# Performance work log

Measured on AMD Instinct MI355X. Metric: run time of the kernel, lower is better.

The kernel has to match this reference:

```python
import jax, jax.numpy as jnp
import numpy as np

EMB_DIM = 1024
HEAD_SIZE = 64
SEQ = 2048
BATCH = 8


def setup_inputs() -> dict:
    key = jax.random.key(0)
    kx, kq, kk, kv = jax.random.split(key, 4)
    x = jax.random.normal(kx, (BATCH, SEQ, EMB_DIM), dtype=jnp.float32)
    # nn.Linear(E, H, bias=False): y = x @ W.T with W of shape [H, E]; store as [E, H]
    s = 1.0 / np.sqrt(EMB_DIM)
    Wq = jax.random.uniform(kq, (EMB_DIM, HEAD_SIZE), jnp.float32, -s, s)
    Wk = jax.random.uniform(kk, (EMB_DIM, HEAD_SIZE), jnp.float32, -s, s)
    Wv = jax.random.uniform(kv, (EMB_DIM, HEAD_SIZE), jnp.float32, -s, s)
    return {"x": x, "Wq": Wq, "Wk": Wk, "Wv": Wv}


def reference(x, Wq, Wk, Wv):
    B, S, E = x.shape
    q = jnp.einsum("bse,eh->bsh", x, Wq)
    k = jnp.einsum("bse,eh->bsh", x, Wk)
    v = jnp.einsum("bse,eh->bsh", x, Wv)
    # NOTE: original scales by E**-0.5 (embedding dim), not head_size**-0.5
    att = jnp.einsum("bqh,bkh->bqk", q, k) * (E ** -0.5)
    causal = jnp.tril(jnp.ones((S, S), dtype=bool))
    att = jnp.where(causal, att, -jnp.inf)
    att = jax.nn.softmax(att, axis=-1)
    # dropout(p=0.2) treated as identity (eval mode) for deterministic reference
    out = jnp.einsum("bqk,bkh->bqh", att, v)
    return out
```

## Files before the change

### kernel.cpp

```cpp
#include <hip/hip_runtime.h>

constexpr int Bn = 8, S = 2048, E = 1024, H = 64;
constexpr float SCALE = 0.03125f * 1.44269504f;

typedef __attribute__((ext_vector_type(8))) short short8;
typedef __attribute__((ext_vector_type(4))) float f32x4;

__device__ __forceinline__ unsigned short f2bf(float f) {
  unsigned u = __builtin_bit_cast(unsigned, f);
  u += 0x7fffu + ((u >> 16) & 1u);
  return (unsigned short)(u >> 16);
}
__device__ __forceinline__ ushort4 f4bf(float4 f) {
  return make_ushort4(f2bf(f.x), f2bf(f.y), f2bf(f.z), f2bf(f.w));
}

__global__ __launch_bounds__(256) void wtrans_kernel(
    const float* __restrict__ Wq, const float* __restrict__ Wk,
    const float* __restrict__ Wv, unsigned short* __restrict__ WT3) {
  __shared__ unsigned short tb[64][72];
  const int m = blockIdx.x >> 4;
  const int e0 = (blockIdx.x & 15) * 64;
  const float* W = (m == 0) ? Wq : (m == 1) ? Wk : Wv;
  const int t = threadIdx.x;
#pragma unroll
  for (int it = 0; it < 4; ++it) {
    int idx = t + it * 256;
    int r = idx >> 4, c4 = idx & 15;
    float4 f = ((const float4*)(W + (long)(e0 + r) * H))[c4];
    *(ushort4*)&tb[r][c4 * 4] = f4bf(f);
  }
  __syncthreads();
#pragma unroll
  for (int it = 0; it < 4; ++it) {
    int idx = t + it * 256;
    int h = idx >> 4, e4 = idx & 15;
    ushort4 u = make_ushort4(tb[e4 * 4 + 0][h], tb[e4 * 4 + 1][h],
                             tb[e4 * 4 + 2][h], tb[e4 * 4 + 3][h]);
    ((ushort4*)(WT3 + (long)(m * 64 + h) * E + e0))[e4] = u;
  }
}

__global__ __launch_bounds__(256) void qkv_kernel(
    const float* __restrict__ x, const unsigned short* __restrict__ WT3,
    unsigned short* __restrict__ q, unsigned short* __restrict__ kk,
    unsigned short* __restrict__ vT) {
  __shared__ unsigned short xs[32][136];
  __shared__ unsigned short ws[192][136];
  const int t = threadIdx.x;
  const int w = t >> 6, lane = t & 63, l15 = lane & 15, g = lane >> 4;
  const long row0 = (long)blockIdx.x * 32;
  const int xrow = t >> 5, xslot = t & 31;
  const int wrow = t >> 4, wslot = t & 15;

  f32x4 acc[2][3];
#pragma unroll
  for (int rt = 0; rt < 2; ++rt)
#pragma unroll
    for (int ct = 0; ct < 3; ++ct) acc[rt][ct] = f32x4{0.f, 0.f, 0.f, 0.f};

  float4 px[4];
  short8 pw[12];
#pragma unroll
  for (int it = 0; it < 4; ++it)
    px[it] = ((const float4*)(x + (row0 + xrow + it * 8) * E))[xslot];
#pragma unroll
  for (int it = 0; it < 12; ++it)
    pw[it] = *(const short8*)(WT3 + (long)(wrow + it * 16) * E + wslot * 8);
#pragma unroll
  for (int it = 0; it < 4; ++it)
    *(ushort4*)&xs[xrow + it * 8][xslot * 4] = f4bf(px[it]);
#pragma unroll
  for (int it = 0; it < 12; ++it)
    *(short8*)&ws[wrow + it * 16][wslot * 8] = pw[it];

  for (int c = 0; c < 8; ++c) {
    __syncthreads();
    if (c < 7) {
      const int e0 = (c + 1) * 128;
#pragma unroll
      for (int it = 0; it < 4; ++it)
        px[it] = ((const float4*)(x + (row0 + xrow + it * 8) * E + e0))[xslot];
#pragma unroll
      for (int it = 0; it < 12; ++it)
        pw[it] = *(const short8*)(WT3 + (long)(wrow + it * 16) * E + e0 + wslot * 8);
    }
#pragma unroll
    for (int kh = 0; kh < 4; ++kh) {
      short8 a0 = *(const short8*)&xs[l15][kh * 32 + g * 8];
      short8 a1 = *(const short8*)&xs[16 + l15][kh * 32 + g * 8];
#pragma unroll
      for (int ct = 0; ct < 3; ++ct) {
        short8 b = *(const short8*)&ws[w * 48 + ct * 16 + l15][kh * 32 + g * 8];
        acc[0][ct] = __builtin_amdgcn_mfma_f32_16x16x32_bf16(a0, b, acc[0][ct], 0, 0, 0);
        acc[1][ct] = __builtin_amdgcn_mfma_f32_16x16x32_bf16(a1, b, acc[1][ct], 0, 0, 0);
      }
    }
    __syncthreads();
    if (c < 7) {
#pragma unroll
      for (int it = 0; it < 4; ++it)
        *(ushort4*)&xs[xrow + it * 8][xslot * 4] = f4bf(px[it]);
#pragma unroll
      for (int it = 0; it < 12; ++it)
        *(short8*)&ws[wrow + it * 16][wslot * 8] = pw[it];
    }
  }

  const int bb = (int)(row0 >> 11);
  const int srow = (int)(row0 & 2047);
#pragma unroll
  for (int ct = 0; ct < 3; ++ct) {
    const int col = w * 48 + ct * 16 + l15;
    const int mm = col >> 6, ch = col & 63;
#pragma unroll
    for (int rt = 0; rt < 2; ++rt) {
      const int srl = rt * 16 + g * 4;
      if (mm == 0) {
#pragma unroll
        for (int r = 0; r < 4; ++r)
          q[(row0 + srl + r) * H + ch] = f2bf(acc[rt][ct][r] * SCALE);
      } else if (mm == 1) {
#pragma unroll
        for (int r = 0; r < 4; ++r)
          kk[(row0 + srl + r) * H + ch] = f2bf(acc[rt][ct][r]);
      } else {
        ushort4 v4 = make_ushort4(f2bf(acc[rt][ct][0]), f2bf(acc[rt][ct][1]),
                                  f2bf(acc[rt][ct][2]), f2bf(acc[rt][ct][3]));
        *(ushort4*)(vT + ((long)bb * H + ch) * S + srow + srl) = v4;
      }
    }
  }
}

__global__ __launch_bounds__(256, 2) void attn_kernel(
    const unsigned short* __restrict__ q, const unsigned short* __restrict__ k,
    const unsigned short* __restrict__ vT, float* __restrict__ out) {
  __shared__ unsigned short pl[4][16][72];
  __shared__ float Om[2][4][64][17];
  __shared__ float ms[2][4][16], ls[2][4][16];
  const int t = threadIdx.x;
  const int w = t >> 6, lane = t & 63, l15 = lane & 15, g = lane >> 4;
  const int b = blockIdx.x & 7, p = blockIdx.x >> 3;
  const unsigned short* kb = k + (long)b * S * H;
  const unsigned short* vb = vT + (long)b * H * S;

  const int qt0 = p, qt1 = 127 - p;
  const int nt0 = (qt0 >> 2) + 1;
  const int nt1 = (qt1 >> 2) + 1;
  const int qtA[2] = {qt0, qt1};
  const int ntA[2] = {nt0, nt1};
  const int k0A[2] = {w, (w + 4 - (nt0 & 3)) & 3};

  short8 bq0[2], bq1[2];
  f32x4 O[2][4];
  float m_[2], l_[2];
#pragma unroll
  for (int ph = 0; ph < 2; ++ph) {
    const unsigned short* qp = q + ((long)b * S + qtA[ph] * 16 + l15) * H + g * 8;
    bq0[ph] = *(const short8*)qp;
    bq1[ph] = *(const short8*)(qp + 32);
    m_[ph] = -1e30f;
    l_[ph] = 0.f;
#pragma unroll
    for (int c = 0; c < 4; ++c) O[ph][c] = f32x4{0.f, 0.f, 0.f, 0.f};
  }

#pragma unroll
  for (int ph = 0; ph < 2; ++ph) {
    const int qrow0 = qtA[ph] * 16;
    const int ntp = ntA[ph];
    short8 ak[4][2];
    int kt = k0A[ph];
    if (kt < ntp) {
#pragma unroll
      for (int c = 0; c < 4; ++c)
#pragma unroll
        for (int kh = 0; kh < 2; ++kh)
          ak[c][kh] = *(const short8*)(kb + (long)(kt * 64 + c * 16 + l15) * H + kh * 32 + g * 8);
    }
    for (; kt < ntp; kt += 4) {
      short8 av[4][2];
#pragma unroll
      for (int c = 0; c < 4; ++c)
#pragma unroll
        for (int kh = 0; kh < 2; ++kh)
          av[c][kh] = *(const short8*)(vb + (long)(c * 16 + l15) * S + kt * 64 + kh * 32 + g * 8);
      f32x4 sc[4];
#pragma unroll
      for (int c = 0; c < 4; ++c) {
        sc[c] = f32x4{0.f, 0.f, 0.f, 0.f};
        sc[c] = __builtin_amdgcn_mfma_f32_16x16x32_bf16(ak[c][0], bq0[ph], sc[c], 0, 0, 0);
        sc[c] = __builtin_amdgcn_mfma_f32_16x16x32_bf16(ak[c][1], bq1[ph], sc[c], 0, 0, 0);
      }
      if (kt + 4 < ntp) {
#pragma unroll
        for (int c = 0; c < 4; ++c)
#pragma unroll
          for (int kh = 0; kh < 2; ++kh)
            ak[c][kh] = *(const short8*)(kb + (long)((kt + 4) * 64 + c * 16 + l15) * H + kh * 32 + g * 8);
      }
      if (kt == ntp - 1) {
#pragma unroll
        for (int c = 0; c < 4; ++c)
#pragma unroll
          for (int r = 0; r < 4; ++r)
            if (kt * 64 + c * 16 + g * 4 + r > qrow0 + l15) sc[c][r] = -1e30f;
      }
      float mx = -1e30f;
#pragma unroll
      for (int c = 0; c < 4; ++c)
#pragma unroll
        for (int r = 0; r < 4; ++r) mx = fmaxf(mx, sc[c][r]);
      mx = fmaxf(mx, __shfl_xor(mx, 16));
      mx = fmaxf(mx, __shfl_xor(mx, 32));
      float mn = fmaxf(m_[ph], mx);
      float al = exp2f(m_[ph] - mn);
      float sum = 0.f;
#pragma unroll
      for (int c = 0; c < 4; ++c)
#pragma unroll
        for (int r = 0; r < 4; ++r) {
          float pe = exp2f(sc[c][r] - mn);
          sc[c][r] = pe;
          sum += pe;
        }
      sum += __shfl_xor(sum, 16);
      sum += __shfl_xor(sum, 32);
      l_[ph] = l_[ph] * al + sum;
      m_[ph] = mn;
#pragma unroll
      for (int c = 0; c < 4; ++c) {
        ushort4 p4 = make_ushort4(f2bf(sc[c][0]), f2bf(sc[c][1]),
                                  f2bf(sc[c][2]), f2bf(sc[c][3]));
        *(ushort4*)&pl[w][l15][c * 16 + g * 4] = p4;
      }
#pragma unroll
      for (int c = 0; c < 4; ++c)
#pragma unroll
        for (int r = 0; r < 4; ++r) O[ph][c][r] *= al;
      short8 bp0 = *(const short8*)&pl[w][l15][g * 8];
      short8 bp1 = *(const short8*)&pl[w][l15][32 + g * 8];
#pragma unroll
      for (int c = 0; c < 4; ++c) {
        O[ph][c] = __builtin_amdgcn_mfma_f32_16x16x32_bf16(av[c][0], bp0, O[ph][c], 0, 0, 0);
        O[ph][c] = __builtin_amdgcn_mfma_f32_16x16x32_bf16(av[c][1], bp1, O[ph][c], 0, 0, 0);
      }
    }
  }

#pragma unroll
  for (int ph = 0; ph < 2; ++ph) {
#pragma unroll
    for (int c = 0; c < 4; ++c)
#pragma unroll
      for (int r = 0; r < 4; ++r)
        Om[ph][w][c * 16 + g * 4 + r][l15] = O[ph][c][r];
    if (g == 0) { ms[ph][w][l15] = m_[ph]; ls[ph][w][l15] = l_[ph]; }
  }
  __syncthreads();
  if (w < 2) {
    const int ph = w;
    float mm0 = ms[ph][0][l15], mm1 = ms[ph][1][l15];
    float mm2 = ms[ph][2][l15], mm3 = ms[ph][3][l15];
    float mstar = fmaxf(fmaxf(mm0, mm1), fmaxf(mm2, mm3));
    float f0 = exp2f(mm0 - mstar), f1 = exp2f(mm1 - mstar);
    float f2 = exp2f(mm2 - mstar), f3 = exp2f(mm3 - mstar);
    float inv = 1.0f / (ls[ph][0][l15] * f0 + ls[ph][1][l15] * f1 +
                        ls[ph][2][l15] * f2 + ls[ph][3][l15] * f3);
    float* op = out + ((long)b * S + qtA[ph] * 16 + l15) * H;
#pragma unroll
    for (int c = 0; c < 4; ++c) {
      float o4[4];
#pragma unroll
      for (int r = 0; r < 4; ++r) {
        const int h = c * 16 + g * 4 + r;
        o4[r] = (Om[ph][0][h][l15] * f0 + Om[ph][1][h][l15] * f1 +
                 Om[ph][2][h][l15] * f2 + Om[ph][3][h][l15] * f3) * inv;
      }
      *(float4*)(op + c * 16 + g * 4) = make_float4(o4[0], o4[1], o4[2], o4[3]);
    }
  }
}

extern "C" void kernel_launch(void* const* d_in, const int* in_sizes, int n_in,
                              void* d_out, int out_size, void* d_ws, size_t ws_size,
                              hipStream_t stream) {
  const float* x  = (const float*)d_in[0];
  const float* Wq = (const float*)d_in[1];
  const float* Wk = (const float*)d_in[2];
  const float* Wv = (const float*)d_in[3];
  float* outp = (float*)d_out;
  unsigned short* WT3 = (unsigned short*)d_ws;
  unsigned short* q  = (unsigned short*)((char*)d_ws + 512 * 1024);
  unsigned short* kk = q + (size_t)Bn * S * H;
  unsigned short* vT = kk + (size_t)Bn * S * H;
  wtrans_kernel<<<dim3(48), dim3(256), 0, stream>>>(Wq, Wk, Wv, WT3);
  qkv_kernel<<<dim3((Bn * S) / 32), dim3(256), 0, stream>>>(x, WT3, q, kk, vT);
  attn_kernel<<<dim3(Bn * 64), dim3(256), 0, stream>>>(q, kk, vT, outp);
}
```

Baseline: 141.4 us.

## Process 32-row query groups per wave to reuse K/V loads, combine via LDS atomics

New measurement: 154.4 us. +9.2%, slower.

```diff
diff --git a/kernel.cpp b/kernel.cpp
--- a/kernel.cpp
+++ b/kernel.cpp
@@ -133,79 +133,78 @@
   }
 }
 
-__global__ __launch_bounds__(256, 2) void attn_kernel(
+__global__ __launch_bounds__(512, 2) void attn_kernel(
     const unsigned short* __restrict__ q, const unsigned short* __restrict__ k,
     const unsigned short* __restrict__ vT, float* __restrict__ out) {
-  __shared__ unsigned short pl[4][16][72];
-  __shared__ float Om[2][4][64][17];
-  __shared__ float ms[2][4][16], ls[2][4][16];
+  __shared__ unsigned short pl[8][16][72];
+  __shared__ float Oacc[2][32][68];
+  __shared__ float ms[2][4][32], ls[2][4][32];
   const int t = threadIdx.x;
   const int w = t >> 6, lane = t & 63, l15 = lane & 15, g = lane >> 4;
+  const int grp = w >> 2, w4 = w & 3;
   const int b = blockIdx.x & 7, p = blockIdx.x >> 3;
+  const int qg = grp ? (63 - p) : p;
+  const int nt = (qg >> 1) + 1;
+  const int qrow0 = qg * 32;
   const unsigned short* kb = k + (long)b * S * H;
   const unsigned short* vb = vT + (long)b * H * S;
 
-  const int qt0 = p, qt1 = 127 - p;
-  const int nt0 = (qt0 >> 2) + 1;
-  const int nt1 = (qt1 >> 2) + 1;
-  const int qtA[2] = {qt0, qt1};
-  const int ntA[2] = {nt0, nt1};
-  const int k0A[2] = {w, (w + 4 - (nt0 & 3)) & 3};
-
-  short8 bq0[2], bq1[2];
+  for (int i = t; i < 2 * 32 * 68; i += 512) ((float*)Oacc)[i] = 0.f;
+
+  short8 bq[2][2];
+#pragma unroll
+  for (int s = 0; s < 2; ++s) {
+    const unsigned short* qp = q + ((long)b * S + qrow0 + s * 16 + l15) * H + g * 8;
+    bq[s][0] = *(const short8*)qp;
+    bq[s][1] = *(const short8*)(qp + 32);
+  }
   f32x4 O[2][4];
-  float m_[2], l_[2];
-#pragma unroll
-  for (int ph = 0; ph < 2; ++ph) {
-    const unsigned short* qp = q + ((long)b * S + qtA[ph] * 16 + l15) * H + g * 8;
-    bq0[ph] = *(const short8*)qp;
-    bq1[ph] = *(const short8*)(qp + 32);
-    m_[ph] = -1e30f;
-    l_[ph] = 0.f;
-#pragma unroll
-    for (int c = 0; c < 4; ++c) O[ph][c] = f32x4{0.f, 0.f, 0.f, 0.f};
-  }
-
-#pragma unroll
-  for (int ph = 0; ph < 2; ++ph) {
-    const int qrow0 = qtA[ph] * 16;
-    const int ntp = ntA[ph];
-    short8 ak[4][2];
-    int kt = k0A[ph];
-    if (kt < ntp) {
-#pragma unroll
-      for (int c = 0; c < 4; ++c)
-#pragma unroll
-        for (int kh = 0; kh < 2; ++kh)
-          ak[c][kh] = *(const short8*)(kb + (long)(kt * 64 + c * 16 + l15) * H + kh * 32 + g * 8);
-    }
-    for (; kt < ntp; kt += 4) {
-      short8 av[4][2];
-#pragma unroll
-      for (int c = 0; c < 4; ++c)
-#pragma unroll
-        for (int kh = 0; kh < 2; ++kh)
-          av[c][kh] = *(const short8*)(vb + (long)(c * 16 + l15) * S + kt * 64 + kh * 32 + g * 8);
+  float m_[2] = {-1e30f, -1e30f}, l_[2] = {0.f, 0.f};
+#pragma unroll
+  for (int s = 0; s < 2; ++s)
+#pragma unroll
+    for (int c = 0; c < 4; ++c) O[s][c] = f32x4{0.f, 0.f, 0.f, 0.f};
+
+  short8 ak[4][2];
+  int kt = w4;
+  if (kt < nt) {
+#pragma unroll
+    for (int c = 0; c < 4; ++c)
+#pragma unroll
+      for (int kh = 0; kh < 2; ++kh)
+        ak[c][kh] = *(const short8*)(kb + (long)(kt * 64 + c * 16 + l15) * H + kh * 32 + g * 8);
+  }
+
+  for (; kt < nt; kt += 4) {
+    short8 av[4][2];
+#pragma unroll
+    for (int c = 0; c < 4; ++c)
+#pragma unroll
+      for (int kh = 0; kh < 2; ++kh)
+        av[c][kh] = *(const short8*)(vb + (long)(c * 16 + l15) * S + kt * 64 + kh * 32 + g * 8);
+    const bool last = (kt == nt - 1);
+#pragma unroll
+    for (int s = 0; s < 2; ++s) {
       f32x4 sc[4];
 #pragma unroll
       for (int c = 0; c < 4; ++c) {
         sc[c] = f32x4{0.f, 0.f, 0.f, 0.f};
-        sc[c] = __builtin_amdgcn_mfma_f32_16x16x32_bf16(ak[c][0], bq0[ph], sc[c], 0, 0, 0);
-        sc[c] = __builtin_amdgcn_mfma_f32_16x16x32_bf16(ak[c][1], bq1[ph], sc[c], 0, 0, 0);
-      }
-      if (kt + 4 < ntp) {
+        sc[c] = __builtin_amdgcn_mfma_f32_16x16x32_bf16(ak[c][0], bq[s][0], sc[c], 0, 0, 0);
+        sc[c] = __builtin_amdgcn_mfma_f32_16x16x32_bf16(ak[c][1], bq[s][1], sc[c], 0, 0, 0);
+      }
+      if (s == 1 && kt + 4 < nt) {
 #pragma unroll
         for (int c = 0; c < 4; ++c)
 #pragma unroll
           for (int kh = 0; kh < 2; ++kh)
             ak[c][kh] = *(const short8*)(kb + (long)((kt + 4) * 64 + c * 16 + l15) * H + kh * 32 + g * 8);
       }
-      if (kt == ntp - 1) {
+      if (last) {
 #pragma unroll
         for (int c = 0; c < 4; ++c)
 #pragma unroll
           for (int r = 0; r < 4; ++r)
-            if (kt * 64 + c * 16 + g * 4 + r > qrow0 + l15) sc[c][r] = -1e30f;
+            if (kt * 64 + c * 16 + g * 4 + r > qrow0 + s * 16 + l15) sc[c][r] = -1e30f;
       }
       float mx = -1e30f;
 #pragma unroll
@@ -214,8 +213,8 @@
         for (int r = 0; r < 4; ++r) mx = fmaxf(mx, sc[c][r]);
       mx = fmaxf(mx, __shfl_xor(mx, 16));
       mx = fmaxf(mx, __shfl_xor(mx, 32));
-      float mn = fmaxf(m_[ph], mx);
-      float al = exp2f(m_[ph] - mn);
+      float mn = fmaxf(m_[s], mx);
+      float al = exp2f(m_[s] - mn);
       float sum = 0.f;
 #pragma unroll
       for (int c = 0; c < 4; ++c)
@@ -227,8 +226,8 @@
         }
       sum += __shfl_xor(sum, 16);
       sum += __shfl_xor(sum, 32);
-      l_[ph] = l_[ph] * al + sum;
-      m_[ph] = mn;
+      l_[s] = l_[s] * al + sum;
+      m_[s] = mn;
 #pragma unroll
       for (int c = 0; c < 4; ++c) {
         ushort4 p4 = make_ushort4(f2bf(sc[c][0]), f2bf(sc[c][1]),
@@ -238,48 +237,56 @@
 #pragma unroll
       for (int c = 0; c < 4; ++c)
 #pragma unroll
-        for (int r = 0; r < 4; ++r) O[ph][c][r] *= al;
+        for (int r = 0; r < 4; ++r) O[s][c][r] *= al;
       short8 bp0 = *(const short8*)&pl[w][l15][g * 8];
       short8 bp1 = *(const short8*)&pl[w][l15][32 + g * 8];
 #pragma unroll
       for (int c = 0; c < 4; ++c) {
-        O[ph][c] = __builtin_amdgcn_mfma_f32_16x16x32_bf16(av[c][0], bp0, O[ph][c], 0, 0, 0);
-        O[ph][c] = __builtin_amdgcn_mfma_f32_16x16x32_bf16(av[c][1], bp1, O[ph][c], 0, 0, 0);
-      }
-    }
-  }
-
-#pragma unroll
-  for (int ph = 0; ph < 2; ++ph) {
+        O[s][c] = __builtin_amdgcn_mfma_f32_16x16x32_bf16(av[c][0], bp0, O[s][c], 0, 0, 0);
+        O[s][c] = __builtin_amdgcn_mfma_f32_16x16x32_bf16(av[c][1], bp1, O[s][c], 0, 0, 0);
+      }
+    }
+  }
+
+  if (g == 0) {
+    ms[grp][w4][l15]      = m_[0];  ls[grp][w4][l15]      = l_[0];
+    ms[grp][w4][16 + l15] = m_[1];  ls[grp][w4][16 + l15] = l_[1];
+  }
+  __syncthreads();
+#pragma unroll
+  for (int s = 0; s < 2; ++s) {
+    const int row = s * 16 + l15;
+    float mm0 = ms[grp][0][row], mm1 = ms[grp][1][row];
+    float mm2 = ms[grp][2][row], mm3 = ms[grp][3][row];
+    float mstar = fmaxf(fmaxf(mm0, mm1), fmaxf(mm2, mm3));
+    float f = exp2f(m_[s] - mstar);
 #pragma unroll
     for (int c = 0; c < 4; ++c)
 #pragma unroll
       for (int r = 0; r < 4; ++r)
-        Om[ph][w][c * 16 + g * 4 + r][l15] = O[ph][c][r];
-    if (g == 0) { ms[ph][w][l15] = m_[ph]; ls[ph][w][l15] = l_[ph]; }
+        atomicAdd(&Oacc[grp][row][c * 16 + g * 4 + r], O[s][c][r] * f);
   }
   __syncthreads();
-  if (w < 2) {
-    const int ph = w;
-    float mm0 = ms[ph][0][l15], mm1 = ms[ph][1][l15];
-    float mm2 = ms[ph][2][l15], mm3 = ms[ph][3][l15];
+  {
+    const int g2 = t >> 8, t256 = t & 255;
+    const int row = t256 >> 3, h0 = (t256 & 7) * 8;
+    const int qgo = g2 ? (63 - p) : p;
+    float mm0 = ms[g2][0][row], mm1 = ms[g2][1][row];
+    float mm2 = ms[g2][2][row], mm3 = ms[g2][3][row];
     float mstar = fmaxf(fmaxf(mm0, mm1), fmaxf(mm2, mm3));
-    float f0 = exp2f(mm0 - mstar), f1 = exp2f(mm1 - mstar);
-    float f2 = exp2f(mm2 - mstar), f3 = exp2f(mm3 - mstar);
-    float inv = 1.0f / (ls[ph][0][l15] * f0 + ls[ph][1][l15] * f1 +
-                        ls[ph][2][l15] * f2 + ls[ph][3][l15] * f3);
-    float* op = out + ((long)b * S + qtA[ph] * 16 + l15) * H;
-#pragma unroll
-    for (int c = 0; c < 4; ++c) {
-      float o4[4];
-#pragma unroll
-      for (int r = 0; r < 4; ++r) {
-        const int h = c * 16 + g * 4 + r;
-        o4[r] = (Om[ph][0][h][l15] * f0 + Om[ph][1][h][l15] * f1 +
-                 Om[ph][2][h][l15] * f2 + Om[ph][3][h][l15] * f3) * inv;
-      }
-      *(float4*)(op + c * 16 + g * 4) = make_float4(o4[0], o4[1], o4[2], o4[3]);
-    }
+    float lsum = ls[g2][0][row] * exp2f(mm0 - mstar) +
+                 ls[g2][1][row] * exp2f(mm1 - mstar) +
+                 ls[g2][2][row] * exp2f(mm2 - mstar) +
+                 ls[g2][3][row] * exp2f(mm3 - mstar);
+    float inv = 1.0f / lsum;
+    float* op = out + ((long)b * S + qgo * 32 + row) * H + h0;
+    float4 o0, o1;
+    o0.x = Oacc[g2][row][h0 + 0] * inv;  o0.y = Oacc[g2][row][h0 + 1] * inv;
+    o0.z = Oacc[g2][row][h0 + 2] * inv;  o0.w = Oacc[g2][row][h0 + 3] * inv;
+    o1.x = Oacc[g2][row][h0 + 4] * inv;  o1.y = Oacc[g2][row][h0 + 5] * inv;
+    o1.z = Oacc[g2][row][h0 + 6] * inv;  o1.w = Oacc[g2][row][h0 + 7] * inv;
+    *(float4*)op = o0;
+    *(float4*)(op + 4) = o1;
   }
 }
 
@@ -297,5 +304,5 @@
   unsigned short* vT = kk + (size_t)Bn * S * H;
   wtrans_kernel<<<dim3(48), dim3(256), 0, stream>>>(Wq, Wk, Wv, WT3);
   qkv_kernel<<<dim3((Bn * S) / 32), dim3(256), 0, stream>>>(x, WT3, q, kk, vT);
-  attn_kernel<<<dim3(Bn * 64), dim3(256), 0, stream>>>(q, kk, vT, outp);
-}
+  attn_kernel<<<dim3(Bn * 32), dim3(512), 0, stream>>>(q, kk, vT, outp);
+}
```
